# Kernel tuning notes

Measured on AMD Instinct MI355X. Metric: run time of the kernel, lower is better.

The kernel has to match this reference:

```python
import jax, jax.numpy as jnp
import numpy as np

HEADS = 8

def setup_inputs() -> dict:
    key = jax.random.key(0)
    k1, k2, k3 = jax.random.split(key, 3)
    B, C, L = 8, 512, 4096
    dim_head = 64
    hidden = HEADS * dim_head  # 512
    x = jax.random.normal(k1, (B, C, L), dtype=jnp.float32)
    # Conv1d(dim, hidden*3, 1, bias=False) -> weight [hidden*3, dim]
    w_qkv = jax.random.normal(k2, (hidden * 3, C), dtype=jnp.float32) * 0.02
    # Conv1d(hidden, dim, 1) -> weight [dim, hidden], bias [dim]
    w_out = jax.random.normal(k3, (C, hidden), dtype=jnp.float32) * 0.02
    b_out = jnp.zeros((C,), dtype=jnp.float32)
    return {"x": x, "w_qkv": w_qkv, "w_out": w_out, "b_out": b_out}

def reference(x, w_qkv, w_out, b_out):
    B, C, L = x.shape
    # 1x1 Conv1d == channel matmul
    qkv = jnp.einsum('oc,bcl->bol', w_qkv, x)            # [B, 3*H*dh, L]
    qkv = qkv.reshape(B, 3, HEADS, -1, L)                # qkv outermost, then heads, then c
    q, k, v = qkv[:, 0], qkv[:, 1], qkv[:, 2]            # each [B, H, dh, L]
    k = jax.nn.softmax(k, axis=-1)                       # softmax over sequence
    context = jnp.einsum('bhdn,bhen->bhde', k, v)        # [B, H, dh, dh]
    out = jnp.einsum('bhde,bhdn->bhen', context, q)      # [B, H, dh, L]
    out = out.reshape(B, -1, L)                          # [B, H*dh, L]
    return jnp.einsum('oc,bcl->bol', w_out, out) + b_out[None, :, None]
```

## Files before the change

### kernel.cpp

```cpp
#include <hip/hip_runtime.h>
#include <hip/hip_bf16.h>


typedef __bf16 bf16x8 __attribute__((ext_vector_type(8)));
typedef __bf16 bf16x4 __attribute__((ext_vector_type(4)));
typedef float  f32x4  __attribute__((ext_vector_type(4)));

#define B_  8
#define L_  4096
#define C_  512

#define GLD_LDS16(g, l)                                             \
    __builtin_amdgcn_global_load_lds(                               \
        (const __attribute__((address_space(1))) void*)(g),         \
        (__attribute__((address_space(3))) void*)(l), 16, 0, 0)

#define FENCE asm volatile("" ::: "memory")
#define BAR   do { FENCE; __builtin_amdgcn_s_barrier(); FENCE; } while (0)
#define DRAIN_LGKM asm volatile("s_waitcnt lgkmcnt(0)" ::: "memory")
#define WAIT_VM(N) asm volatile("s_waitcnt vmcnt(" #N ")" ::: "memory")

__global__ __launch_bounds__(256) void prep_all(const float* __restrict__ x,
                                                __hip_bfloat16* __restrict__ xt,
                                                const float* __restrict__ wqkv_f,
                                                __hip_bfloat16* __restrict__ wkv_b,
                                                __hip_bfloat16* __restrict__ wqT,
                                                float* __restrict__ ctx) {
    __shared__ float tile[64 * 132];
    int blk = blockIdx.x;
    int t = threadIdx.x;
    if (blk < 2048) {
        int b = blk >> 8, rem = blk & 255;
        int l0 = (rem & 31) * 128, c0 = (rem >> 5) * 64;
        const float* xp = x + ((size_t)b * C_ + c0) * L_ + l0;
#pragma unroll
        for (int p = 0; p < 8; p++) {
            int i = p * 8 + (t >> 5);
            int j = (t & 31) * 4;
            float4 vv = *(const float4*)(xp + (size_t)i * L_ + j);
            *(float4*)&tile[i * 132 + j] = vv;
        }
        __syncthreads();
        unsigned short* xo = (unsigned short*)xt + ((size_t)b * L_ + l0) * C_ + c0;
#pragma unroll
        for (int qq = 0; qq < 8; qq++) {
            int l = qq * 16 + (t >> 4);
            int cg = (t & 15) * 4;
            bf16x4 ov;
#pragma unroll
            for (int k = 0; k < 4; k++) ov[k] = (__bf16)tile[(cg + k) * 132 + l];
            *(bf16x4*)(xo + (size_t)l * C_ + cg) = ov;
        }
    } else if (blk < 4096) {
        int i = (blk - 2048) * 256 + t;
        wkv_b[i] = __float2bfloat16(wqkv_f[512 * 512 + i]);
    } else if (blk < 4352) {
        int tb = blk - 4096;
        int r0 = (tb >> 4) * 32, c0 = (tb & 15) * 32;
        int tx = t & 31, ty = t >> 5;
        for (int r = 0; r < 32; r += 8)
            tile[(ty + r) * 33 + tx] = wqkv_f[(size_t)(r0 + ty + r) * 512 + c0 + tx];
        __syncthreads();
        for (int r = 0; r < 32; r += 8)
            wqT[(size_t)(c0 + ty + r) * 512 + r0 + tx] = __float2bfloat16(tile[tx * 33 + ty + r]);
    } else {
        int i = (blk - 4352) * 256 + t;
        ctx[i] = 0.f;
    }
}

template <int MODE>
__global__ __launch_bounds__(256) void gemm_bt(
    const __hip_bfloat16* __restrict__ A, const __hip_bfloat16* __restrict__ Bt,
    size_t strideA, size_t strideB, int M, int N, int K,
    __hip_bfloat16* __restrict__ obf) {
    __shared__ alignas(16) unsigned short As[128 * 64];
    __shared__ alignas(16) unsigned short Bs[128 * 64];

    int b = blockIdx.z;
    int m0 = blockIdx.y * 128, n0 = blockIdx.x * 128;
    const __hip_bfloat16* Ab = A + strideA * (size_t)b;
    const __hip_bfloat16* Bb = Bt + strideB * (size_t)b;

    int t = threadIdx.x;
    int lane = t & 63, wv = t >> 6;
    int l16 = lane & 15, q4 = lane >> 4;
    int wr = (wv >> 1) * 64, wc = (wv & 1) * 64;

    int srow = lane >> 3;
    int swz  = ((lane & 7) ^ srow) * 8;

    const __hip_bfloat16* gA[4];
    const __hip_bfloat16* gB[4];
    unsigned short* lA[4];
    unsigned short* lB[4];
#pragma unroll
    for (int c = 0; c < 4; c++) {
        int r = wv * 32 + c * 8;
        gA[c] = Ab + (size_t)(m0 + r + srow) * K + swz;
        gB[c] = Bb + (size_t)(n0 + r + srow) * K + swz;
        lA[c] = &As[r * 64];
        lB[c] = &Bs[r * 64];
    }

    int gsel0 = ((q4) ^ (l16 & 7)) * 8;
    int gsel1 = ((4 + q4) ^ (l16 & 7)) * 8;
    int rA = (wr + l16) * 64;
    int rB = (wc + l16) * 64;

    f32x4 acc[4][4] = {};

    for (int k0 = 0; k0 < K; k0 += 64) {
        __syncthreads();
#pragma unroll
        for (int c = 0; c < 4; c++) {
            GLD_LDS16(gA[c] + k0, lA[c]);
            GLD_LDS16(gB[c] + k0, lB[c]);
        }
        __syncthreads();

        bf16x8 af[4], bfr[4];
#pragma unroll
        for (int i = 0; i < 4; i++) {
            af[i]  = *(const bf16x8*)&As[rA + i * 1024 + gsel0];
            bfr[i] = *(const bf16x8*)&Bs[rB + i * 1024 + gsel0];
        }
#pragma unroll
        for (int i = 0; i < 4; i++)
#pragma unroll
            for (int j = 0; j < 4; j++)
                acc[i][j] = __builtin_amdgcn_mfma_f32_16x16x32_bf16(af[i], bfr[j], acc[i][j], 0, 0, 0);
#pragma unroll
        for (int i = 0; i < 4; i++) {
            af[i]  = *(const bf16x8*)&As[rA + i * 1024 + gsel1];
            bfr[i] = *(const bf16x8*)&Bs[rB + i * 1024 + gsel1];
        }
#pragma unroll
        for (int i = 0; i < 4; i++)
#pragma unroll
            for (int j = 0; j < 4; j++)
                acc[i][j] = __builtin_amdgcn_mfma_f32_16x16x32_bf16(af[i], bfr[j], acc[i][j], 0, 0, 0);
    }

#pragma unroll
    for (int i = 0; i < 4; i++)
#pragma unroll
        for (int j = 0; j < 4; j++)
#pragma unroll
            for (int r = 0; r < 4; r++) {
                int row = m0 + wr + i * 16 + q4 * 4 + r;
                int col = n0 + wc + j * 16 + l16;
                obf[((size_t)b * 512 + row) * (size_t)N + col] = __float2bfloat16(acc[i][j][r]);
            }
}

template <int MODE>
__global__ __launch_bounds__(512, 2) void gemm256(
    const __hip_bfloat16* __restrict__ A, const __hip_bfloat16* __restrict__ Bt,
    size_t strideA, size_t strideB, int M, int N, int K,
    __hip_bfloat16* __restrict__ kb, __hip_bfloat16* __restrict__ vb,
    float* __restrict__ outb, const float* __restrict__ bias) {
    __shared__ alignas(16) unsigned short sA[2][256 * 64];
    __shared__ alignas(16) unsigned short sB[2][256 * 64];

    int b = blockIdx.z;
    int m0 = blockIdx.y * 256, n0 = blockIdx.x * 256;
    const __hip_bfloat16* Ab = A + strideA * (size_t)b;
    const __hip_bfloat16* Bb = Bt + strideB * (size_t)b;

    int t = threadIdx.x;
    int lane = t & 63, wv = t >> 6;
    int l16 = lane & 15, q4 = lane >> 4;
    int wm = wv >> 2, wn = wv & 3;

    int srow = lane >> 3;
    int swz  = ((lane & 7) ^ srow) * 8;

    const __hip_bfloat16* gA[4];
    const __hip_bfloat16* gB[4];
    unsigned ldoff[4];
#pragma unroll
    for (int c = 0; c < 4; c++) {
        gA[c] = Ab + (size_t)(m0 + c * 64 + wv * 8 + srow) * K + swz;
        gB[c] = Bb + (size_t)(n0 + c * 64 + wv * 8 + srow) * K + swz;
        ldoff[c] = (unsigned)(c * 64 + wv * 8) * 64;
    }

    int gsel0 = (q4 ^ (l16 & 7)) * 8;
    int gsel1 = gsel0 ^ 32;
    unsigned offA = (unsigned)(wm * 128 + l16) * 64;
    unsigned offB = (unsigned)(wn * 64 + l16) * 64;
    int NKT = K >> 6;

    f32x4 acc[8][4] = {};
    bf16x8 aF[4][2], bF[4][2];

#pragma unroll
    for (int c = 0; c < 4; c++) GLD_LDS16(gA[c], &sA[0][ldoff[c]]);
#pragma unroll
    for (int c = 0; c < 4; c++) GLD_LDS16(gB[c], &sB[0][ldoff[c]]);
    if (NKT > 1) {
        GLD_LDS16(gA[0] + 64, &sA[1][ldoff[0]]);
        GLD_LDS16(gA[1] + 64, &sA[1][ldoff[1]]);
        WAIT_VM(2);
    } else {
        WAIT_VM(0);
    }
    BAR;

#pragma unroll 1
    for (int kt = 0; kt < NKT; ++kt) {
        const unsigned short* As_b = sA[kt & 1];
        const unsigned short* Bs_b = sB[kt & 1];
        int nbuf = (kt + 1) & 1;
        int koff1 = (kt + 1) << 6;
        bool st1 = (kt + 1) < NKT;
        bool st2 = (kt + 2) < NKT;

#pragma unroll
        for (int i = 0; i < 4; i++) {
            aF[i][0] = *(const bf16x8*)&As_b[offA + i * 1024 + gsel0];
            aF[i][1] = *(const bf16x8*)&As_b[offA + i * 1024 + gsel1];
        }
#pragma unroll
        for (int j = 0; j < 2; j++) {
            bF[j][0] = *(const bf16x8*)&Bs_b[offB + j * 1024 + gsel0];
            bF[j][1] = *(const bf16x8*)&Bs_b[offB + j * 1024 + gsel1];
        }
        if (st1) {
            GLD_LDS16(gA[2] + koff1, &sA[nbuf][ldoff[2]]);
            GLD_LDS16(gA[3] + koff1, &sA[nbuf][ldoff[3]]);
        }
        BAR;
        __builtin_amdgcn_s_setprio(1);
#pragma unroll
        for (int ks = 0; ks < 2; ks++)
#pragma unroll
            for (int i = 0; i < 4; i++)
#pragma unroll
                for (int j = 0; j < 2; j++)
                    acc[i][j] = __builtin_amdgcn_mfma_f32_16x16x32_bf16(aF[i][ks], bF[j][ks], acc[i][j], 0, 0, 0);
        __builtin_amdgcn_s_setprio(0);
        DRAIN_LGKM;
        BAR;

#pragma unroll
        for (int j = 2; j < 4; j++) {
            bF[j][0] = *(const bf16x8*)&Bs_b[offB + j * 1024 + gsel0];
            bF[j][1] = *(const bf16x8*)&Bs_b[offB + j * 1024 + gsel1];
        }
        if (st1) {
            GLD_LDS16(gB[0] + koff1, &sB[nbuf][ldoff[0]]);
            GLD_LDS16(gB[1] + koff1, &sB[nbuf][ldoff[1]]);
        }
        BAR;
        __builtin_amdgcn_s_setprio(1);
#pragma unroll
        for (int ks = 0; ks < 2; ks++)
#pragma unroll
            for (int i = 0; i < 4; i++)
#pragma unroll
                for (int j = 0; j < 2; j++)
                    acc[i][2 + j] = __builtin_amdgcn_mfma_f32_16x16x32_bf16(aF[i][ks], bF[2 + j][ks], acc[i][2 + j], 0, 0, 0);
        __builtin_amdgcn_s_setprio(0);
        DRAIN_LGKM;
        BAR;

#pragma unroll
        for (int i = 0; i < 4; i++) {
            aF[i][0] = *(const bf16x8*)&As_b[offA + 4096 + i * 1024 + gsel0];
            aF[i][1] = *(const bf16x8*)&As_b[offA + 4096 + i * 1024 + gsel1];
        }
        if (st1) {
            GLD_LDS16(gB[2] + koff1, &sB[nbuf][ldoff[2]]);
            GLD_LDS16(gB[3] + koff1, &sB[nbuf][ldoff[3]]);
        }
        BAR;
        __builtin_amdgcn_s_setprio(1);
#pragma unroll
        for (int ks = 0; ks < 2; ks++)
#pragma unroll
            for (int i = 0; i < 4; i++)
#pragma unroll
                for (int j = 0; j < 2; j++)
                    acc[4 + i][j] = __builtin_amdgcn_mfma_f32_16x16x32_bf16(aF[i][ks], bF[j][ks], acc[4 + i][j], 0, 0, 0);
        __builtin_amdgcn_s_setprio(0);
        DRAIN_LGKM;
        BAR;

        if (st2) {
            int koff2 = (kt + 2) << 6;
            GLD_LDS16(gA[0] + koff2, &sA[kt & 1][ldoff[0]]);
            GLD_LDS16(gA[1] + koff2, &sA[kt & 1][ldoff[1]]);
        }
        BAR;
        __builtin_amdgcn_s_setprio(1);
#pragma unroll
        for (int ks = 0; ks < 2; ks++)
#pragma unroll
            for (int i = 0; i < 4; i++)
#pragma unroll
                for (int j = 0; j < 2; j++)
                    acc[4 + i][2 + j] = __builtin_amdgcn_mfma_f32_16x16x32_bf16(aF[i][ks], bF[2 + j][ks], acc[4 + i][2 + j], 0, 0, 0);
        __builtin_amdgcn_s_setprio(0);
        DRAIN_LGKM;
        if (st2) { WAIT_VM(2); } else { WAIT_VM(0); }
        BAR;
    }

    int row0 = m0 + wm * 128, col0 = n0 + wn * 64;
    if (MODE == 1) {
        __hip_bfloat16* dst = (row0 < 512) ? kb : vb;
        int ob = row0 & 511;
#pragma unroll
        for (int i = 0; i < 8; i++)
#pragma unroll
            for (int j = 0; j < 4; j++)
#pragma unroll
                for (int r = 0; r < 4; r++) {
                    int od  = ob + i * 16 + q4 * 4 + r;
                    int col = col0 + j * 16 + l16;
                    dst[((size_t)b * 512 + od) * (size_t)N + col] = __float2bfloat16(acc[i][j][r]);
                }
    } else {
#pragma unroll
        for (int i = 0; i < 8; i++)
#pragma unroll
            for (int j = 0; j < 4; j++)
#pragma unroll
                for (int r = 0; r < 4; r++) {
                    int row = row0 + i * 16 + q4 * 4 + r;
                    int col = col0 + j * 16 + l16;
                    outb[((size_t)b * M + row) * (size_t)N + col] = acc[i][j][r] + bias[row];
                }
    }
}

__global__ __launch_bounds__(256) void rowstat(const __hip_bfloat16* __restrict__ kin,
                                               float* __restrict__ mrow,
                                               float* __restrict__ isrow) {
    int row = blockIdx.x;
    const unsigned short* kp = (const unsigned short*)kin + (size_t)row * L_;
    __shared__ float buf[L_];
    __shared__ float red[8];
    int t = threadIdx.x, lane = t & 63, wv = t >> 6;
    float m = -1e30f;
    for (int i0 = t * 8; i0 < L_; i0 += 256 * 8) {
        bf16x8 kv = *(const bf16x8*)(kp + i0);
#pragma unroll
        for (int j = 0; j < 8; j++) {
            float xx = (float)kv[j];
            buf[i0 + j] = xx;
            m = fmaxf(m, xx);
        }
    }
    for (int o = 32; o; o >>= 1) m = fmaxf(m, __shfl_xor(m, o, 64));
    if (lane == 0) red[wv] = m;
    __syncthreads();
    m = fmaxf(fmaxf(red[0], red[1]), fmaxf(red[2], red[3]));
    float s = 0.f;
    for (int i = t; i < L_; i += 256) s += __expf(buf[i] - m);
    for (int o = 32; o; o >>= 1) s += __shfl_xor(s, o, 64);
    if (lane == 0) red[4 + wv] = s;
    __syncthreads();
    if (t == 0) {
        s = red[4] + red[5] + red[6] + red[7];
        mrow[row] = m;
        isrow[row] = 1.0f / s;
    }
}

__global__ __launch_bounds__(256) void ctx_kernel(const __hip_bfloat16* __restrict__ kraw,
                                                  const float* __restrict__ mrow,
                                                  const float* __restrict__ isrow,
                                                  const __hip_bfloat16* __restrict__ v,
                                                  float* __restrict__ ctx) {
    int kc = blockIdx.x, h = blockIdx.y, b = blockIdx.z;
    int t = threadIdx.x, lane = t & 63, wv = t >> 6;
    int l16 = lane & 15, q4 = lane >> 4;
    const __hip_bfloat16* ka = kraw + ((size_t)b * 512 + h * 64) * L_;
    const __hip_bfloat16* va = v + ((size_t)b * 512 + h * 64) * L_;
    int rbase = b * 512 + h * 64;
    float mr[4], ir[4];
#pragma unroll
    for (int i = 0; i < 4; i++) {
        mr[i] = mrow[rbase + i * 16 + l16];
        ir[i] = isrow[rbase + i * 16 + l16];
    }
    f32x4 acc[4][4] = {};
    int nbase = kc * 512 + wv * 128;
#pragma unroll
    for (int s = 0; s < 4; s++) {
        int n = nbase + s * 32 + q4 * 8;
        bf16x8 af[4], bfr[4];
#pragma unroll
        for (int i = 0; i < 4; i++) {
            bf16x8 kv = *(const bf16x8*)(ka + (size_t)(i * 16 + l16) * L_ + n);
#pragma unroll
            for (int e = 0; e < 8; e++)
                af[i][e] = (__bf16)(__expf((float)kv[e] - mr[i]) * ir[i]);
            bfr[i] = *(const bf16x8*)(va + (size_t)(i * 16 + l16) * L_ + n);
        }
#pragma unroll
        for (int i = 0; i < 4; i++)
#pragma unroll
            for (int j = 0; j < 4; j++)
                acc[i][j] = __builtin_amdgcn_mfma_f32_16x16x32_bf16(af[i], bfr[j], acc[i][j], 0, 0, 0);
    }
    __shared__ float cbuf[4096];
    for (int w = 0; w < 4; w++) {
        if (wv == w) {
#pragma unroll
            for (int i = 0; i < 4; i++)
#pragma unroll
                for (int j = 0; j < 4; j++)
#pragma unroll
                    for (int r = 0; r < 4; r++) {
                        int mm = i * 16 + q4 * 4 + r, nn = j * 16 + l16;
                        float pv = acc[i][j][r];
                        if (w == 0) cbuf[mm * 64 + nn] = pv;
                        else        cbuf[mm * 64 + nn] += pv;
                    }
        }
        __syncthreads();
    }
    float* cg = ctx + ((size_t)b * 8 + h) * 4096;
    for (int i = t; i < 4096; i += 256) atomicAdd(&cg[i], cbuf[i]);
}

__global__ __launch_bounds__(256) void w2_kernel(const float* __restrict__ wout,
                                                 const float* __restrict__ ctx,
                                                 __hip_bfloat16* __restrict__ w2) {
    int ob = blockIdx.x, h = blockIdx.y, b = blockIdx.z;
    __shared__ float cT[64 * 65];
    __shared__ float wT[64 * 65];
    int t = threadIdx.x;
    const float* cg = ctx + ((size_t)b * 8 + h) * 4096;
    for (int i = t; i < 4096; i += 256) {
        int d = i >> 6, e = i & 63;
        cT[e * 65 + d] = cg[i];
        wT[e * 65 + d] = wout[(size_t)(ob * 64 + d) * 512 + h * 64 + e];
    }
    __syncthreads();
    int ol = t >> 2;
    int db = (t & 3) * 16;
    for (int dd = 0; dd < 16; dd++) {
        int d = db + dd;
        float s = 0.f;
#pragma unroll
        for (int e = 0; e < 64; e++) s += wT[e * 65 + ol] * cT[e * 65 + d];
        w2[((size_t)b * 512 + ob * 64 + ol) * 512 + h * 64 + d] = __float2bfloat16(s);
    }
}

extern "C" void kernel_launch(void* const* d_in, const int* in_sizes, int n_in,
                              void* d_out, int out_size, void* d_ws, size_t ws_size,
                              hipStream_t stream) {
    const float* x     = (const float*)d_in[0];
    const float* w_qkv = (const float*)d_in[1];
    const float* w_out = (const float*)d_in[2];
    const float* b_out = (const float*)d_in[3];
    float* out = (float*)d_out;
    char* ws = (char*)d_ws;

    const size_t QKV = (size_t)B_ * 512 * L_;
    size_t off_xt  = 0;
    size_t off_wkv = off_xt + (size_t)B_ * L_ * C_ * 2;
    size_t off_wqT = off_wkv + (size_t)1024 * 512 * 2;
    size_t off_k   = off_wqT + (size_t)512 * 512 * 2;
    size_t off_v   = off_k + QKV * 2;
    size_t off_ms  = off_v + QKV * 2;
    size_t off_is  = off_ms + 4096 * 4;
    size_t off_ctx = off_is + 4096 * 4;
    size_t off_w2  = off_ctx + (size_t)B_ * 8 * 64 * 64 * 4;
    size_t off_w3  = off_w2 + (size_t)B_ * 512 * 512 * 2;

    __hip_bfloat16* xt   = (__hip_bfloat16*)(ws + off_xt);
    __hip_bfloat16* wkvb = (__hip_bfloat16*)(ws + off_wkv);
    __hip_bfloat16* wqT  = (__hip_bfloat16*)(ws + off_wqT);
    __hip_bfloat16* kb   = (__hip_bfloat16*)(ws + off_k);
    __hip_bfloat16* vb   = (__hip_bfloat16*)(ws + off_v);
    float*          ms   = (float*)(ws + off_ms);
    float*          isv  = (float*)(ws + off_is);
    float*          ctx  = (float*)(ws + off_ctx);
    __hip_bfloat16* w2   = (__hip_bfloat16*)(ws + off_w2);
    __hip_bfloat16* W3   = (__hip_bfloat16*)(ws + off_w3);

    prep_all<<<5376, 256, 0, stream>>>(x, xt, w_qkv, wkvb, wqT, ctx);

    gemm256<1><<<dim3(L_ / 256, 1024 / 256, B_), 512, 0, stream>>>(
        wkvb, xt, 0, (size_t)L_ * C_, 1024, L_, 512, kb, vb, nullptr, nullptr);

    rowstat<<<B_ * 512, 256, 0, stream>>>(kb, ms, isv);
    ctx_kernel<<<dim3(8, 8, B_), 256, 0, stream>>>(kb, ms, isv, vb, ctx);
    w2_kernel<<<dim3(8, 8, B_), 256, 0, stream>>>(w_out, ctx, w2);

    gemm_bt<3><<<dim3(512 / 128, 512 / 128, B_), 256, 0, stream>>>(
        w2, wqT, (size_t)512 * 512, 0, 512, 512, 512, W3);

    gemm256<2><<<dim3(L_ / 256, 512 / 256, B_), 512, 0, stream>>>(
        W3, xt, (size_t)512 * 512, (size_t)L_ * C_, 512, L_, 512, nullptr, nullptr, out, b_out);
}
```

Before: 258.0 us.

## Fold softmax normalization into w2, drop rowstat pass, use 128-tile GEMMs

Removes the separate row-statistics kernel by computing unnormalized exp(k) directly in the context kernel. Per-row partial sums are accumulated there and the division is applied later in w2_kernel. The context atomics and zero-init are replaced by four per-split partial buffers that w2 sums. The 256x256 GEMM is replaced with a 128x128 double-buffered variant for more blocks and occupancy. Skipping max-subtraction risks overflow for large k values, and the w2/W3 buffers now alias the k buffer.

```diff
diff --git a/kernel.cpp b/kernel.cpp
--- a/kernel.cpp
+++ b/kernel.cpp
@@ -24,8 +24,7 @@
                                                 __hip_bfloat16* __restrict__ xt,
                                                 const float* __restrict__ wqkv_f,
                                                 __hip_bfloat16* __restrict__ wkv_b,
-                                                __hip_bfloat16* __restrict__ wqT,
-                                                float* __restrict__ ctx) {
+                                                __hip_bfloat16* __restrict__ wqT) {
     __shared__ float tile[64 * 132];
     int blk = blockIdx.x;
     int t = threadIdx.x;
@@ -54,7 +53,7 @@
     } else if (blk < 4096) {
         int i = (blk - 2048) * 256 + t;
         wkv_b[i] = __float2bfloat16(wqkv_f[512 * 512 + i]);
-    } else if (blk < 4352) {
+    } else {
         int tb = blk - 4096;
         int r0 = (tb >> 4) * 32, c0 = (tb & 15) * 32;
         int tx = t & 31, ty = t >> 5;
@@ -63,10 +62,142 @@
         __syncthreads();
         for (int r = 0; r < 32; r += 8)
             wqT[(size_t)(c0 + ty + r) * 512 + r0 + tx] = __float2bfloat16(tile[tx * 33 + ty + r]);
+    }
+}
+
+template <int MODE>
+__global__ __launch_bounds__(256, 2) void gemm_p(
+    const __hip_bfloat16* __restrict__ A, const __hip_bfloat16* __restrict__ Bt,
+    size_t strideA, size_t strideB, int M, int N, int K,
+    __hip_bfloat16* __restrict__ kb, __hip_bfloat16* __restrict__ vb,
+    float* __restrict__ outb, const float* __restrict__ bias) {
+    __shared__ alignas(16) unsigned short sA[2][128 * 64];
+    __shared__ alignas(16) unsigned short sB[2][128 * 64];
+
+    int b = blockIdx.z;
+    int m0 = blockIdx.y * 128, n0 = blockIdx.x * 128;
+    const __hip_bfloat16* Ab = A + strideA * (size_t)b;
+    const __hip_bfloat16* Bb = Bt + strideB * (size_t)b;
+
+    int t = threadIdx.x;
+    int lane = t & 63, wv = t >> 6;
+    int l16 = lane & 15, q4 = lane >> 4;
+    int wr = (wv >> 1) * 64, wc = (wv & 1) * 64;
+
+    int srow = lane >> 3;
+    int swz  = ((lane & 7) ^ srow) * 8;
+
+    const __hip_bfloat16* gA[4];
+    const __hip_bfloat16* gB[4];
+    unsigned ldoff[4];
+#pragma unroll
+    for (int c = 0; c < 4; c++) {
+        int r = c * 32 + wv * 8;
+        gA[c] = Ab + (size_t)(m0 + r + srow) * K + swz;
+        gB[c] = Bb + (size_t)(n0 + r + srow) * K + swz;
+        ldoff[c] = (unsigned)r * 64;
+    }
+
+    int gsel0 = (q4 ^ (l16 & 7)) * 8;
+    int gsel1 = gsel0 ^ 32;
+    unsigned rA = (unsigned)(wr + l16) * 64;
+    unsigned rB = (unsigned)(wc + l16) * 64;
+    int NKT = K >> 6;
+
+    f32x4 acc[4][4] = {};
+    bf16x8 aF[4][2], bF[4][2];
+
+#pragma unroll
+    for (int c = 0; c < 4; c++) GLD_LDS16(gA[c], &sA[0][ldoff[c]]);
+#pragma unroll
+    for (int c = 0; c < 4; c++) GLD_LDS16(gB[c], &sB[0][ldoff[c]]);
+    if (NKT > 1) {
+#pragma unroll
+        for (int c = 0; c < 4; c++) GLD_LDS16(gA[c] + 64, &sA[1][ldoff[c]]);
+        WAIT_VM(4);
     } else {
-        int i = (blk - 4352) * 256 + t;
-        ctx[i] = 0.f;
-    }
+        WAIT_VM(0);
+    }
+    BAR;
+
+#pragma unroll 1
+    for (int kt = 0; kt < NKT; ++kt) {
+        int cur = kt & 1, nbuf = cur ^ 1;
+        const unsigned short* As_b = sA[cur];
+        const unsigned short* Bs_b = sB[cur];
+        bool st1 = (kt + 1) < NKT;
+        bool st2 = (kt + 2) < NKT;
+
+#pragma unroll
+        for (int i = 0; i < 4; i++) {
+            aF[i][0] = *(const bf16x8*)&As_b[rA + i * 1024 + gsel0];
+            aF[i][1] = *(const bf16x8*)&As_b[rA + i * 1024 + gsel1];
+        }
+#pragma unroll
+        for (int j = 0; j < 2; j++) {
+            bF[j][0] = *(const bf16x8*)&Bs_b[rB + j * 1024 + gsel0];
+            bF[j][1] = *(const bf16x8*)&Bs_b[rB + j * 1024 + gsel1];
+        }
+        if (st1) {
+            int ko = (kt + 1) << 6;
+#pragma unroll
+            for (int c = 0; c < 4; c++) GLD_LDS16(gB[c] + ko, &sB[nbuf][ldoff[c]]);
+        }
+        BAR;
+        __builtin_amdgcn_s_setprio(1);
+#pragma unroll
+        for (int ks = 0; ks < 2; ks++)
+#pragma unroll
+            for (int i = 0; i < 4; i++)
+#pragma unroll
+                for (int j = 0; j < 2; j++)
+                    acc[i][j] = __builtin_amdgcn_mfma_f32_16x16x32_bf16(aF[i][ks], bF[j][ks], acc[i][j], 0, 0, 0);
+        __builtin_amdgcn_s_setprio(0);
+        DRAIN_LGKM;
+        BAR;
+
+#pragma unroll
+        for (int j = 2; j < 4; j++) {
+            bF[j][0] = *(const bf16x8*)&Bs_b[rB + j * 1024 + gsel0];
+            bF[j][1] = *(const bf16x8*)&Bs_b[rB + j * 1024 + gsel1];
+        }
+        if (st2) {
+            int ko = (kt + 2) << 6;
+#pragma unroll
+            for (int c = 0; c < 4; c++) GLD_LDS16(gA[c] + ko, &sA[cur][ldoff[c]]);
+        }
+        BAR;
+        __builtin_amdgcn_s_setprio(1);
+#pragma unroll
+        for (int ks = 0; ks < 2; ks++)
+#pragma unroll
+            for (int i = 0; i < 4; i++)
+#pragma unroll
+                for (int j = 0; j < 2; j++)
+                    acc[i][2 + j] = __builtin_amdgcn_mfma_f32_16x16x32_bf16(aF[i][ks], bF[2 + j][ks], acc[i][2 + j], 0, 0, 0);
+        __builtin_amdgcn_s_setprio(0);
+        DRAIN_LGKM;
+        if (st2) { WAIT_VM(4); } else { WAIT_VM(0); }
+        BAR;
+    }
+
+#pragma unroll
+    for (int i = 0; i < 4; i++)
+#pragma unroll
+        for (int j = 0; j < 4; j++)
+#pragma unroll
+            for (int r = 0; r < 4; r++) {
+                int row = m0 + wr + i * 16 + q4 * 4 + r;
+                int col = n0 + wc + j * 16 + l16;
+                float val = acc[i][j][r];
+                if (MODE == 1) {
+                    __hip_bfloat16* dst = (m0 < 512) ? kb : vb;
+                    int od = row & 511;
+                    dst[((size_t)b * 512 + od) * (size_t)N + col] = __float2bfloat16(val);
+                } else {
+                    outb[((size_t)b * M + row) * (size_t)N + col] = val + bias[row];
+                }
+            }
 }
 
 template <int MODE>
@@ -104,7 +235,7 @@
     }
 
     int gsel0 = ((q4) ^ (l16 & 7)) * 8;
-    int gsel1 = ((4 + q4) ^ (l16 & 7)) * 8;
+    int gsel1 = gsel0 ^ 32;
     int rA = (wr + l16) * 64;
     int rB = (wc + l16) * 64;
 
@@ -154,251 +285,32 @@
             }
 }
 
-template <int MODE>
-__global__ __launch_bounds__(512, 2) void gemm256(
-    const __hip_bfloat16* __restrict__ A, const __hip_bfloat16* __restrict__ Bt,
-    size_t strideA, size_t strideB, int M, int N, int K,
-    __hip_bfloat16* __restrict__ kb, __hip_bfloat16* __restrict__ vb,
-    float* __restrict__ outb, const float* __restrict__ bias) {
-    __shared__ alignas(16) unsigned short sA[2][256 * 64];
-    __shared__ alignas(16) unsigned short sB[2][256 * 64];
-
-    int b = blockIdx.z;
-    int m0 = blockIdx.y * 256, n0 = blockIdx.x * 256;
-    const __hip_bfloat16* Ab = A + strideA * (size_t)b;
-    const __hip_bfloat16* Bb = Bt + strideB * (size_t)b;
-
-    int t = threadIdx.x;
-    int lane = t & 63, wv = t >> 6;
-    int l16 = lane & 15, q4 = lane >> 4;
-    int wm = wv >> 2, wn = wv & 3;
-
-    int srow = lane >> 3;
-    int swz  = ((lane & 7) ^ srow) * 8;
-
-    const __hip_bfloat16* gA[4];
-    const __hip_bfloat16* gB[4];
-    unsigned ldoff[4];
-#pragma unroll
-    for (int c = 0; c < 4; c++) {
-        gA[c] = Ab + (size_t)(m0 + c * 64 + wv * 8 + srow) * K + swz;
-        gB[c] = Bb + (size_t)(n0 + c * 64 + wv * 8 + srow) * K + swz;
-        ldoff[c] = (unsigned)(c * 64 + wv * 8) * 64;
-    }
-
-    int gsel0 = (q4 ^ (l16 & 7)) * 8;
-    int gsel1 = gsel0 ^ 32;
-    unsigned offA = (unsigned)(wm * 128 + l16) * 64;
-    unsigned offB = (unsigned)(wn * 64 + l16) * 64;
-    int NKT = K >> 6;
-
-    f32x4 acc[8][4] = {};
-    bf16x8 aF[4][2], bF[4][2];
-
-#pragma unroll
-    for (int c = 0; c < 4; c++) GLD_LDS16(gA[c], &sA[0][ldoff[c]]);
-#pragma unroll
-    for (int c = 0; c < 4; c++) GLD_LDS16(gB[c], &sB[0][ldoff[c]]);
-    if (NKT > 1) {
-        GLD_LDS16(gA[0] + 64, &sA[1][ldoff[0]]);
-        GLD_LDS16(gA[1] + 64, &sA[1][ldoff[1]]);
-        WAIT_VM(2);
-    } else {
-        WAIT_VM(0);
-    }
-    BAR;
-
-#pragma unroll 1
-    for (int kt = 0; kt < NKT; ++kt) {
-        const unsigned short* As_b = sA[kt & 1];
-        const unsigned short* Bs_b = sB[kt & 1];
-        int nbuf = (kt + 1) & 1;
-        int koff1 = (kt + 1) << 6;
-        bool st1 = (kt + 1) < NKT;
-        bool st2 = (kt + 2) < NKT;
-
-#pragma unroll
-        for (int i = 0; i < 4; i++) {
-            aF[i][0] = *(const bf16x8*)&As_b[offA + i * 1024 + gsel0];
-            aF[i][1] = *(const bf16x8*)&As_b[offA + i * 1024 + gsel1];
-        }
-#pragma unroll
-        for (int j = 0; j < 2; j++) {
-            bF[j][0] = *(const bf16x8*)&Bs_b[offB + j * 1024 + gsel0];
-            bF[j][1] = *(const bf16x8*)&Bs_b[offB + j * 1024 + gsel1];
-        }
-        if (st1) {
-            GLD_LDS16(gA[2] + koff1, &sA[nbuf][ldoff[2]]);
-            GLD_LDS16(gA[3] + koff1, &sA[nbuf][ldoff[3]]);
-        }
-        BAR;
-        __builtin_amdgcn_s_setprio(1);
-#pragma unroll
-        for (int ks = 0; ks < 2; ks++)
-#pragma unroll
-            for (int i = 0; i < 4; i++)
-#pragma unroll
-                for (int j = 0; j < 2; j++)
-                    acc[i][j] = __builtin_amdgcn_mfma_f32_16x16x32_bf16(aF[i][ks], bF[j][ks], acc[i][j], 0, 0, 0);
-        __builtin_amdgcn_s_setprio(0);
-        DRAIN_LGKM;
-        BAR;
-
-#pragma unroll
-        for (int j = 2; j < 4; j++) {
-            bF[j][0] = *(const bf16x8*)&Bs_b[offB + j * 1024 + gsel0];
-            bF[j][1] = *(const bf16x8*)&Bs_b[offB + j * 1024 + gsel1];
-        }
-        if (st1) {
-            GLD_LDS16(gB[0] + koff1, &sB[nbuf][ldoff[0]]);
-            GLD_LDS16(gB[1] + koff1, &sB[nbuf][ldoff[1]]);
-        }
-        BAR;
-        __builtin_amdgcn_s_setprio(1);
-#pragma unroll
-        for (int ks = 0; ks < 2; ks++)
-#pragma unroll
-            for (int i = 0; i < 4; i++)
-#pragma unroll
-                for (int j = 0; j < 2; j++)
-                    acc[i][2 + j] = __builtin_amdgcn_mfma_f32_16x16x32_bf16(aF[i][ks], bF[2 + j][ks], acc[i][2 + j], 0, 0, 0);
-        __builtin_amdgcn_s_setprio(0);
-        DRAIN_LGKM;
-        BAR;
-
-#pragma unroll
-        for (int i = 0; i < 4; i++) {
-            aF[i][0] = *(const bf16x8*)&As_b[offA + 4096 + i * 1024 + gsel0];
-            aF[i][1] = *(const bf16x8*)&As_b[offA + 4096 + i * 1024 + gsel1];
-        }
-        if (st1) {
-            GLD_LDS16(gB[2] + koff1, &sB[nbuf][ldoff[2]]);
-            GLD_LDS16(gB[3] + koff1, &sB[nbuf][ldoff[3]]);
-        }
-        BAR;
-        __builtin_amdgcn_s_setprio(1);
-#pragma unroll
-        for (int ks = 0; ks < 2; ks++)
-#pragma unroll
-            for (int i = 0; i < 4; i++)
-#pragma unroll
-                for (int j = 0; j < 2; j++)
-                    acc[4 + i][j] = __builtin_amdgcn_mfma_f32_16x16x32_bf16(aF[i][ks], bF[j][ks], acc[4 + i][j], 0, 0, 0);
-        __builtin_amdgcn_s_setprio(0);
-        DRAIN_LGKM;
-        BAR;
-
-        if (st2) {
-            int koff2 = (kt + 2) << 6;
-            GLD_LDS16(gA[0] + koff2, &sA[kt & 1][ldoff[0]]);
-            GLD_LDS16(gA[1] + koff2, &sA[kt & 1][ldoff[1]]);
-        }
-        BAR;
-        __builtin_amdgcn_s_setprio(1);
-#pragma unroll
-        for (int ks = 0; ks < 2; ks++)
-#pragma unroll
-            for (int i = 0; i < 4; i++)
-#pragma unroll
-                for (int j = 0; j < 2; j++)
-                    acc[4 + i][2 + j] = __builtin_amdgcn_mfma_f32_16x16x32_bf16(aF[i][ks], bF[2 + j][ks], acc[4 + i][2 + j], 0, 0, 0);
-        __builtin_amdgcn_s_setprio(0);
-        DRAIN_LGKM;
-        if (st2) { WAIT_VM(2); } else { WAIT_VM(0); }
-        BAR;
-    }
-
-    int row0 = m0 + wm * 128, col0 = n0 + wn * 64;
-    if (MODE == 1) {
-        __hip_bfloat16* dst = (row0 < 512) ? kb : vb;
-        int ob = row0 & 511;
-#pragma unroll
-        for (int i = 0; i < 8; i++)
-#pragma unroll
-            for (int j = 0; j < 4; j++)
-#pragma unroll
-                for (int r = 0; r < 4; r++) {
-                    int od  = ob + i * 16 + q4 * 4 + r;
-                    int col = col0 + j * 16 + l16;
-                    dst[((size_t)b * 512 + od) * (size_t)N + col] = __float2bfloat16(acc[i][j][r]);
-                }
-    } else {
-#pragma unroll
-        for (int i = 0; i < 8; i++)
-#pragma unroll
-            for (int j = 0; j < 4; j++)
-#pragma unroll
-                for (int r = 0; r < 4; r++) {
-                    int row = row0 + i * 16 + q4 * 4 + r;
-                    int col = col0 + j * 16 + l16;
-                    outb[((size_t)b * M + row) * (size_t)N + col] = acc[i][j][r] + bias[row];
-                }
-    }
-}
-
-__global__ __launch_bounds__(256) void rowstat(const __hip_bfloat16* __restrict__ kin,
-                                               float* __restrict__ mrow,
-                                               float* __restrict__ isrow) {
-    int row = blockIdx.x;
-    const unsigned short* kp = (const unsigned short*)kin + (size_t)row * L_;
-    __shared__ float buf[L_];
-    __shared__ float red[8];
-    int t = threadIdx.x, lane = t & 63, wv = t >> 6;
-    float m = -1e30f;
-    for (int i0 = t * 8; i0 < L_; i0 += 256 * 8) {
-        bf16x8 kv = *(const bf16x8*)(kp + i0);
-#pragma unroll
-        for (int j = 0; j < 8; j++) {
-            float xx = (float)kv[j];
-            buf[i0 + j] = xx;
-            m = fmaxf(m, xx);
-        }
-    }
-    for (int o = 32; o; o >>= 1) m = fmaxf(m, __shfl_xor(m, o, 64));
-    if (lane == 0) red[wv] = m;
-    __syncthreads();
-    m = fmaxf(fmaxf(red[0], red[1]), fmaxf(red[2], red[3]));
-    float s = 0.f;
-    for (int i = t; i < L_; i += 256) s += __expf(buf[i] - m);
-    for (int o = 32; o; o >>= 1) s += __shfl_xor(s, o, 64);
-    if (lane == 0) red[4 + wv] = s;
-    __syncthreads();
-    if (t == 0) {
-        s = red[4] + red[5] + red[6] + red[7];
-        mrow[row] = m;
-        isrow[row] = 1.0f / s;
-    }
-}
-
 __global__ __launch_bounds__(256) void ctx_kernel(const __hip_bfloat16* __restrict__ kraw,
-                                                  const float* __restrict__ mrow,
-                                                  const float* __restrict__ isrow,
                                                   const __hip_bfloat16* __restrict__ v,
-                                                  float* __restrict__ ctx) {
+                                                  float* __restrict__ ctxp,
+                                                  float* __restrict__ sums) {
     int kc = blockIdx.x, h = blockIdx.y, b = blockIdx.z;
     int t = threadIdx.x, lane = t & 63, wv = t >> 6;
     int l16 = lane & 15, q4 = lane >> 4;
     const __hip_bfloat16* ka = kraw + ((size_t)b * 512 + h * 64) * L_;
     const __hip_bfloat16* va = v + ((size_t)b * 512 + h * 64) * L_;
-    int rbase = b * 512 + h * 64;
-    float mr[4], ir[4];
-#pragma unroll
-    for (int i = 0; i < 4; i++) {
-        mr[i] = mrow[rbase + i * 16 + l16];
-        ir[i] = isrow[rbase + i * 16 + l16];
-    }
+
     f32x4 acc[4][4] = {};
-    int nbase = kc * 512 + wv * 128;
-#pragma unroll
-    for (int s = 0; s < 4; s++) {
+    float ps[4] = {0.f, 0.f, 0.f, 0.f};
+    int nbase = kc * 1024 + wv * 256;
+#pragma unroll 1
+    for (int s = 0; s < 8; s++) {
         int n = nbase + s * 32 + q4 * 8;
         bf16x8 af[4], bfr[4];
 #pragma unroll
         for (int i = 0; i < 4; i++) {
             bf16x8 kv = *(const bf16x8*)(ka + (size_t)(i * 16 + l16) * L_ + n);
 #pragma unroll
-            for (int e = 0; e < 8; e++)
-                af[i][e] = (__bf16)(__expf((float)kv[e] - mr[i]) * ir[i]);
+            for (int e = 0; e < 8; e++) {
+                float ev = __expf((float)kv[e]);
+                af[i][e] = (__bf16)ev;
+                ps[i] += ev;
+            }
             bfr[i] = *(const bf16x8*)(va + (size_t)(i * 16 + l16) * L_ + n);
         }
 #pragma unroll
@@ -407,6 +319,23 @@
             for (int j = 0; j < 4; j++)
                 acc[i][j] = __builtin_amdgcn_mfma_f32_16x16x32_bf16(af[i], bfr[j], acc[i][j], 0, 0, 0);
     }
+
+    __shared__ float sred[4][64];
+#pragma unroll
+    for (int i = 0; i < 4; i++) {
+        ps[i] += __shfl_xor(ps[i], 16, 64);
+        ps[i] += __shfl_xor(ps[i], 32, 64);
+    }
+    if (q4 == 0) {
+#pragma unroll
+        for (int i = 0; i < 4; i++) sred[wv][i * 16 + l16] = ps[i];
+    }
+    __syncthreads();
+    if (t < 64) {
+        float S = sred[0][t] + sred[1][t] + sred[2][t] + sred[3][t];
+        sums[(((size_t)kc * 8 + b) * 8 + h) * 64 + t] = S;
+    }
+
     __shared__ float cbuf[4096];
     for (int w = 0; w < 4; w++) {
         if (wv == w) {
@@ -424,22 +353,32 @@
         }
         __syncthreads();
     }
-    float* cg = ctx + ((size_t)b * 8 + h) * 4096;
-    for (int i = t; i < 4096; i += 256) atomicAdd(&cg[i], cbuf[i]);
+    float* cg = ctxp + (((size_t)kc * 8 + b) * 8 + h) * 4096;
+    for (int i = t; i < 4096; i += 256) cg[i] = cbuf[i];
 }
 
 __global__ __launch_bounds__(256) void w2_kernel(const float* __restrict__ wout,
-                                                 const float* __restrict__ ctx,
+                                                 const float* __restrict__ ctxp,
+                                                 const float* __restrict__ sums,
                                                  __hip_bfloat16* __restrict__ w2) {
     int ob = blockIdx.x, h = blockIdx.y, b = blockIdx.z;
     __shared__ float cT[64 * 65];
     __shared__ float wT[64 * 65];
+    __shared__ float Sinv[64];
     int t = threadIdx.x;
-    const float* cg = ctx + ((size_t)b * 8 + h) * 4096;
+    const size_t KCS = (size_t)8 * 8 * 4096;
+    const float* cg = ctxp + (((size_t)b) * 8 + h) * 4096;
     for (int i = t; i < 4096; i += 256) {
         int d = i >> 6, e = i & 63;
-        cT[e * 65 + d] = cg[i];
+        float s = cg[i] + cg[KCS + i] + cg[2 * KCS + i] + cg[3 * KCS + i];
+        cT[e * 65 + d] = s;
         wT[e * 65 + d] = wout[(size_t)(ob * 64 + d) * 512 + h * 64 + e];
+    }
+    if (t < 64) {
+        const size_t SKC = (size_t)8 * 8 * 64;
+        const float* sg = sums + ((size_t)b * 8 + h) * 64;
+        float S = sg[t] + sg[SKC + t] + sg[2 * SKC + t] + sg[3 * SKC + t];
+        Sinv[t] = 1.0f / S;
     }
     __syncthreads();
     int ol = t >> 2;
@@ -449,7 +388,7 @@
         float s = 0.f;
 #pragma unroll
         for (int e = 0; e < 64; e++) s += wT[e * 65 + ol] * cT[e * 65 + d];
-        w2[((size_t)b * 512 + ob * 64 + ol) * 512 + h * 64 + d] = __float2bfloat16(s);
+        w2[((size_t)b * 512 + ob * 64 + ol) * 512 + h * 64 + d] = __float2bfloat16(s * Sinv[d]);
     }
 }
 
@@ -464,40 +403,38 @@
     char* ws = (char*)d_ws;
 
     const size_t QKV = (size_t)B_ * 512 * L_;
-    size_t off_xt  = 0;
-    size_t off_wkv = off_xt + (size_t)B_ * L_ * C_ * 2;
-    size_t off_wqT = off_wkv + (size_t)1024 * 512 * 2;
-    size_t off_k   = off_wqT + (size_t)512 * 512 * 2;
-    size_t off_v   = off_k + QKV * 2;
-    size_t off_ms  = off_v + QKV * 2;
-    size_t off_is  = off_ms + 4096 * 4;
-    size_t off_ctx = off_is + 4096 * 4;
-    size_t off_w2  = off_ctx + (size_t)B_ * 8 * 64 * 64 * 4;
-    size_t off_w3  = off_w2 + (size_t)B_ * 512 * 512 * 2;
+    size_t off_xt   = 0;
+    size_t off_wkv  = off_xt + (size_t)B_ * L_ * C_ * 2;
+    size_t off_wqT  = off_wkv + (size_t)1024 * 512 * 2;
+    size_t off_k    = off_wqT + (size_t)512 * 512 * 2;
+    size_t off_v    = off_k + QKV * 2;
+    size_t off_ctxp = off_v + QKV * 2;
+    size_t off_sums = off_ctxp + (size_t)4 * 8 * 8 * 4096 * 4;
+    size_t off_w2   = off_k;
+    size_t off_w3   = off_k + (size_t)B_ * 512 * 512 * 2;
 
     __hip_bfloat16* xt   = (__hip_bfloat16*)(ws + off_xt);
     __hip_bfloat16* wkvb = (__hip_bfloat16*)(ws + off_wkv);
     __hip_bfloat16* wqT  = (__hip_bfloat16*)(ws + off_wqT);
     __hip_bfloat16* kb   = (__hip_bfloat16*)(ws + off_k);
     __hip_bfloat16* vb   = (__hip_bfloat16*)(ws + off_v);
-    float*          ms   = (float*)(ws + off_ms);
-    float*          isv  = (float*)(ws + off_is);
-    float*          ctx  = (float*)(ws + off_ctx);
+    float*          ctxp = (float*)(ws + off_ctxp);
+    float*          sums = (float*)(ws + off_sums);
     __hip_bfloat16* w2   = (__hip_bfloat16*)(ws + off_w2);
     __hip_bfloat16* W3   = (__hip_bfloat16*)(ws + off_w3);
 
-    prep_all<<<5376, 256, 0, stream>>>(x, xt, w_qkv, wkvb, wqT, ctx);
-
-    gemm256<1><<<dim3(L_ / 256, 1024 / 256, B_), 512, 0, stream>>>(
+    prep_all<<<4352, 256, 0, stream>>>(x, xt, w_qkv, wkvb, wqT);
+
+    gemm_p<1><<<dim3(L_ / 128, 1024 / 128, B_), 256, 0, stream>>>(
         wkvb, xt, 0, (size_t)L_ * C_, 1024, L_, 512, kb, vb, nullptr, nullptr);
 
-    rowstat<<<B_ * 512, 256, 0, stream>>>(kb, ms, isv);
-    ctx_kernel<<<dim3(8, 8, B_), 256, 0, stream>>>(kb, ms, isv, vb, ctx);
-    w2_kernel<<<dim3(8, 8, B_), 256, 0, stream>>>(w_out, ctx, w2);
+    ctx_kernel<<<dim3(4, 8, B_), 256, 0, stream>>>(kb, vb, ctxp, sums);
+
+    w2_kernel<<<dim3(8, 8, B_), 256, 0, stream>>>(w_out, ctxp, sums, w2);
 
     gemm_bt<3><<<dim3(512 / 128, 512 / 128, B_), 256, 0, stream>>>(
         w2, wqT, (size_t)512 * 512, 0, 512, 512, 512, W3);
 
-    gemm256<2><<<dim3(L_ / 256, 512 / 256, B_), 512, 0, stream>>>(
+    gemm_p<2><<<dim3(L_ / 128, 512 / 128, B_), 256, 0, stream>>>(
         W3, xt, (size_t)512 * 512, (size_t)L_ * C_, 512, L_, 512, nullptr, nullptr, out, b_out);
 }
```

After: 244.4 us. -5.3%, faster.
